# Performance work log

Hardware: AMD Instinct MI355X
Metric: run time of the kernel (lower is better)

Reference implementation:

```python
import jax, jax.numpy as jnp
import numpy as np

HEAD_DIM = 128
N = 64  # board_size**2


def setup_inputs() -> dict:
    key = jax.random.key(0)
    ks = jax.random.split(key, 14)
    B, C = 64, 256
    d = HEAD_DIM
    sc_conv = (2.0 / d) ** 0.5          # kaiming fan_out for 1x1 conv (fan_out = out_ch)
    inp = {
        'x': jax.random.normal(ks[0], (B, C, 8, 8), dtype=jnp.float32),
        # 1x1 convs stored as [out, in] matrices
        'w_src': jax.random.normal(ks[1], (d, C), dtype=jnp.float32) * sc_conv,
        'b_src': jax.random.normal(ks[2], (d,), dtype=jnp.float32) * 0.01,
        'w_dst': jax.random.normal(ks[3], (d, C), dtype=jnp.float32) * sc_conv,
        'b_dst': jax.random.normal(ks[4], (d,), dtype=jnp.float32) * 0.01,
        'w_arr': jax.random.normal(ks[5], (d, C), dtype=jnp.float32) * sc_conv,
        'b_arr': jax.random.normal(ks[6], (d,), dtype=jnp.float32) * 0.01,
        # move_fusion MLP: Linear(256,256) -> ReLU -> Linear(256,128) -> ReLU -> Linear(128,128)
        'w1': jax.random.normal(ks[7], (2 * d, 2 * d), dtype=jnp.float32) * (2.0 / (2 * d)) ** 0.5,
        'b1': jnp.zeros((2 * d,), dtype=jnp.float32),
        'w2': jax.random.normal(ks[8], (d, 2 * d), dtype=jnp.float32) * (2.0 / d) ** 0.5,
        'b2': jnp.zeros((d,), dtype=jnp.float32),
        'w3': jax.random.normal(ks[9], (d, d), dtype=jnp.float32) * (2.0 / d) ** 0.5,
        'b3': jnp.zeros((d,), dtype=jnp.float32),
    }
    return inp


def reference(x, w_src, b_src, w_dst, b_dst, w_arr, b_arr, w1, b1, w2, b2, w3, b3):
    B, C, H, W = x.shape
    d = HEAD_DIM
    scale = 1.0 / d ** 0.5
    xf = x.reshape(B, C, N)                                   # B,C,64
    f_src = jnp.einsum('oc,bcn->bon', w_src, xf) + b_src[:, None]  # B,128,64
    f_dst = jnp.einsum('oc,bcn->bon', w_dst, xf) + b_dst[:, None]
    f_arr = jnp.einsum('oc,bcn->bon', w_arr, xf) + b_arr[:, None]

    q_src = jnp.transpose(f_src, (0, 2, 1))                   # B,N,128
    move_logits = jnp.einsum('bnd,bdm->bnm', q_src, f_dst) * scale  # B,N,N

    # Linear(cat([v_src, v_dst])) decomposed: v@W1^T = src@W1[:, :d]^T + dst@W1[:, d:]^T
    dst_t = jnp.transpose(f_dst, (0, 2, 1))                   # B,N,128
    src_p = jnp.einsum('bnd,hd->bnh', q_src, w1[:, :d])       # B,N,256
    dst_p = jnp.einsum('bmd,hd->bmh', dst_t, w1[:, d:])       # B,N,256
    h1 = jax.nn.relu(src_p[:, :, None, :] + dst_p[:, None, :, :] + b1)  # B,N,N,256
    h2 = jax.nn.relu(jnp.einsum('bnmh,oh->bnmo', h1, w2) + b2)          # B,N,N,128
    q = jnp.einsum('bnmo,po->bnmp', h2, w3) + b3                        # B,N,N,128
    arrow_logits = jnp.einsum('bnmd,bdk->bnmk', q, f_arr).reshape(B, N * N, N) * scale
    return (move_logits, arrow_logits)
```

## Files before the change

### kernel.cpp

```cpp
#include <hip/hip_runtime.h>
#include <hip/hip_bf16.h>
#include <cstdint>

#define DEV __device__ __forceinline__

typedef __bf16 bf16_t;
typedef __bf16 bf16x8 __attribute__((ext_vector_type(8)));
typedef __bf16 bf16x4 __attribute__((ext_vector_type(4)));
typedef float  f32x4  __attribute__((ext_vector_type(4)));

constexpr float SCALE = 0.08838834764831845f;

constexpr size_t OFF_WSRC = 0;
constexpr size_t OFF_WDST = 65536;
constexpr size_t OFF_WARR = 131072;
constexpr size_t OFF_W1   = 196608;
constexpr size_t OFF_W2   = 327680;
constexpr size_t OFF_W3T  = 393216;
constexpr size_t OFF_FT   = 425984;
constexpr size_t OFF_GT   = OFF_FT + 3u*1048576u;
constexpr size_t OFF_C    = OFF_GT + 1048576u;
constexpr size_t OFF_SP   = OFF_C + 16384u;
constexpr size_t OFF_DP   = OFF_SP + 4194304u;

DEV f32x4 mfma16(bf16x8 a, bf16x8 b, f32x4 c) {
  return __builtin_amdgcn_mfma_f32_16x16x32_bf16(a, b, c, 0, 0, 0);
}

DEV bf16x8 lds_ld8(const bf16_t* base, int row, int k, int ldaBytes) {
  int off = (row * ldaBytes + k * 2) ^ ((row & 7) << 4);
  return *(const bf16x8*)((const char*)base + off);
}
DEV void lds_st8(bf16_t* base, int row, int k, int ldaBytes, bf16x8 v) {
  int off = (row * ldaBytes + k * 2) ^ ((row & 7) << 4);
  *(bf16x8*)((char*)base + off) = v;
}
DEV void lds_st4(bf16_t* base, int row, int k, int ldaBytes, bf16x4 v) {
  int off = (row * ldaBytes + k * 2) ^ ((row & 7) << 4);
  *(bf16x4*)((char*)base + off) = v;
}
DEV void lds_st1(bf16_t* base, int row, int k, int ldaBytes, bf16_t v) {
  int off = (row * ldaBytes + k * 2) ^ ((row & 7) << 4);
  *(bf16_t*)((char*)base + off) = v;
}
DEV bf16x8 g_ld8(const bf16_t* p) { return *(const bf16x8*)p; }

__global__ __launch_bounds__(256) void k0_prep(
    const float* __restrict__ wsrc, const float* __restrict__ wdst,
    const float* __restrict__ warr, const float* __restrict__ w1,
    const float* __restrict__ w2, const float* __restrict__ w3,
    char* __restrict__ ws)
{
  int tid = blockIdx.x * 256 + threadIdx.x;
  int stride = gridDim.x * 256;
  bf16_t* osrc = (bf16_t*)(ws + OFF_WSRC);
  bf16_t* odst = (bf16_t*)(ws + OFF_WDST);
  bf16_t* oarr = (bf16_t*)(ws + OFF_WARR);
  bf16_t* ow1  = (bf16_t*)(ws + OFF_W1);
  bf16_t* ow2  = (bf16_t*)(ws + OFF_W2);
  bf16_t* ow3t = (bf16_t*)(ws + OFF_W3T);
  for (int i = tid; i < 32768; i += stride) {
    osrc[i] = (bf16_t)wsrc[i];
    odst[i] = (bf16_t)wdst[i];
    oarr[i] = (bf16_t)warr[i];
    ow2[i]  = (bf16_t)w2[i];
  }
  for (int i = tid; i < 65536; i += stride) ow1[i] = (bf16_t)w1[i];
  for (int i = tid; i < 16384; i += stride) {
    int o = i >> 7, p = i & 127;
    ow3t[i] = (bf16_t)w3[p * 128 + o];
  }
}

__global__ __launch_bounds__(256) void k1_fproj(
    const float* __restrict__ x,
    const float* __restrict__ bsrc, const float* __restrict__ bdst,
    const float* __restrict__ barr, char* __restrict__ ws)
{
  int X = blockIdx.x % 3, b = blockIdx.x / 3;
  __shared__ __attribute__((aligned(16))) bf16_t xfT[64 * 256];

  int t = threadIdx.x;
  const float* xb = x + (size_t)b * 16384;
  #pragma unroll
  for (int i = 0; i < 16; i++) {
    int idx4 = (i * 256 + t) * 4;
    int c = idx4 >> 6, p = idx4 & 63;
    f32x4 v = *(const f32x4*)(xb + idx4);
    #pragma unroll
    for (int j = 0; j < 4; j++) lds_st1(xfT, p + j, c, 512, (bf16_t)v[j]);
  }
  __syncthreads();

  const bf16_t* wb = (const bf16_t*)(ws + OFF_WSRC + (size_t)X * 65536);
  const float* bias = (X == 0) ? bsrc : ((X == 1) ? bdst : barr);
  bf16_t* fT = (bf16_t*)(ws + OFF_FT + (size_t)X * 1048576u + (size_t)b * 16384u);

  int lane = t & 63, wave = t >> 6, r16 = lane & 15, g = lane >> 4;
  f32x4 z = {0.f, 0.f, 0.f, 0.f};
  f32x4 acc[2][4];
  #pragma unroll
  for (int rf = 0; rf < 2; rf++)
    #pragma unroll
    for (int cf = 0; cf < 4; cf++) acc[rf][cf] = z;

  #pragma unroll
  for (int ks = 0; ks < 8; ks++) {
    int k = ks * 32 + g * 8;
    bf16x8 a[2], bb[4];
    #pragma unroll
    for (int rf = 0; rf < 2; rf++)
      a[rf] = g_ld8(wb + (wave * 32 + rf * 16 + r16) * 256 + k);
    #pragma unroll
    for (int cf = 0; cf < 4; cf++) bb[cf] = lds_ld8(xfT, cf * 16 + r16, k, 512);
    __builtin_amdgcn_s_setprio(1);
    #pragma unroll
    for (int rf = 0; rf < 2; rf++)
      #pragma unroll
      for (int cf = 0; cf < 4; cf++) acc[rf][cf] = mfma16(a[rf], bb[cf], acc[rf][cf]);
    __builtin_amdgcn_s_setprio(0);
  }
  #pragma unroll
  for (int rf = 0; rf < 2; rf++) {
    int o0 = wave * 32 + rf * 16 + g * 4;
    f32x4 bv = *(const f32x4*)(bias + o0);
    #pragma unroll
    for (int cf = 0; cf < 4; cf++) {
      int p = cf * 16 + r16;
      bf16x4 pk;
      #pragma unroll
      for (int j = 0; j < 4; j++) pk[j] = (bf16_t)(acc[rf][cf][j] + bv[j]);
      *(bf16x4*)(fT + p * 128 + o0) = pk;
    }
  }
}

__global__ __launch_bounds__(256) void k2_pre(
    const float* __restrict__ b1, const float* __restrict__ b3,
    char* __restrict__ ws, float* __restrict__ out)
{
  int b = blockIdx.x & 63, task = blockIdx.x >> 6;
  int t = threadIdx.x, lane = t & 63, wave = t >> 6, r16 = lane & 15, g = lane >> 4;
  const bf16_t* fsrcT = (const bf16_t*)(ws + OFF_FT) + (size_t)b * 8192;
  const bf16_t* fdstT = (const bf16_t*)(ws + OFF_FT + 1048576u) + (size_t)b * 8192;
  const bf16_t* farrT = (const bf16_t*)(ws + OFF_FT + 2097152u) + (size_t)b * 8192;
  f32x4 z = {0.f, 0.f, 0.f, 0.f};

  if (task == 0) {
    f32x4 acc[4];
    #pragma unroll
    for (int cf = 0; cf < 4; cf++) acc[cf] = z;
    #pragma unroll
    for (int ks = 0; ks < 4; ks++) {
      int k = ks * 32 + g * 8;
      bf16x8 bb = g_ld8(fsrcT + (wave * 16 + r16) * 128 + k);
      #pragma unroll
      for (int cf = 0; cf < 4; cf++) {
        bf16x8 a = g_ld8(fdstT + (cf * 16 + r16) * 128 + k);
        acc[cf] = mfma16(a, bb, acc[cf]);
      }
    }
    float* ob = out + (size_t)b * 4096;
    int n = wave * 16 + r16;
    #pragma unroll
    for (int cf = 0; cf < 4; cf++) {
      f32x4 v;
      #pragma unroll
      for (int j = 0; j < 4; j++) v[j] = acc[cf][j] * SCALE;
      *(f32x4*)(ob + n * 64 + cf * 16 + g * 4) = v;
    }
  } else if (task <= 2) {
    const bf16_t* Bm = (const bf16_t*)(ws + OFF_W1) + (size_t)(wave * 64) * 256 + (task == 2 ? 128 : 0);
    const bf16_t* A = (task == 1) ? fsrcT : fdstT;
    f32x4 acc[4][4];
    #pragma unroll
    for (int cf = 0; cf < 4; cf++)
      #pragma unroll
      for (int rf = 0; rf < 4; rf++) acc[cf][rf] = z;
    #pragma unroll
    for (int ks = 0; ks < 4; ks++) {
      int k = ks * 32 + g * 8;
      bf16x8 aw[4], bb[4];
      #pragma unroll
      for (int cf = 0; cf < 4; cf++) aw[cf] = g_ld8(Bm + (cf * 16 + r16) * 256 + k);
      #pragma unroll
      for (int rf = 0; rf < 4; rf++) bb[rf] = g_ld8(A + (rf * 16 + r16) * 128 + k);
      __builtin_amdgcn_s_setprio(1);
      #pragma unroll
      for (int cf = 0; cf < 4; cf++)
        #pragma unroll
        for (int rf = 0; rf < 4; rf++) acc[cf][rf] = mfma16(aw[cf], bb[rf], acc[cf][rf]);
      __builtin_amdgcn_s_setprio(0);
    }
    if (task == 1) {
      float* sp = (float*)(ws + OFF_SP) + (size_t)b * 16384;
      #pragma unroll
      for (int cf = 0; cf < 4; cf++) {
        int h0 = wave * 64 + cf * 16 + g * 4;
        f32x4 bv = *(const f32x4*)(b1 + h0);
        #pragma unroll
        for (int rf = 0; rf < 4; rf++) {
          int n = rf * 16 + r16;
          *(f32x4*)(sp + n * 256 + h0) = acc[cf][rf] + bv;
        }
      }
    } else {
      bf16_t* dpo = (bf16_t*)(ws + OFF_DP) + (size_t)b * 16384;
      #pragma unroll
      for (int cf = 0; cf < 4; cf++) {
        int h0 = wave * 64 + cf * 16 + g * 4;
        #pragma unroll
        for (int rf = 0; rf < 4; rf++) {
          int m = rf * 16 + r16;
          bf16x4 pk;
          #pragma unroll
          for (int j = 0; j < 4; j++) pk[j] = (bf16_t)acc[cf][rf][j];
          *(bf16x4*)(dpo + m * 256 + h0) = pk;
        }
      }
    }
  } else {
    const bf16_t* A = (const bf16_t*)(ws + OFF_W3T) + (size_t)(wave * 32) * 128;
    f32x4 acc[2][4];
    #pragma unroll
    for (int rf = 0; rf < 2; rf++)
      #pragma unroll
      for (int cf = 0; cf < 4; cf++) acc[rf][cf] = z;
    #pragma unroll
    for (int ks = 0; ks < 4; ks++) {
      int k = ks * 32 + g * 8;
      bf16x8 a[2], bb[4];
      #pragma unroll
      for (int rf = 0; rf < 2; rf++) a[rf] = g_ld8(A + (rf * 16 + r16) * 128 + k);
      #pragma unroll
      for (int cf = 0; cf < 4; cf++) bb[cf] = g_ld8(farrT + (cf * 16 + r16) * 128 + k);
      #pragma unroll
      for (int rf = 0; rf < 2; rf++)
        #pragma unroll
        for (int cf = 0; cf < 4; cf++) acc[rf][cf] = mfma16(a[rf], bb[cf], acc[rf][cf]);
    }
    bf16_t* GT = (bf16_t*)(ws + OFF_GT) + (size_t)b * 8192;
    #pragma unroll
    for (int rf = 0; rf < 2; rf++) {
      int o0 = wave * 32 + rf * 16 + g * 4;
      #pragma unroll
      for (int cf = 0; cf < 4; cf++) {
        int kc = cf * 16 + r16;
        bf16x4 pk;
        #pragma unroll
        for (int j = 0; j < 4; j++) pk[j] = (bf16_t)(acc[rf][cf][j] * SCALE);
        *(bf16x4*)(GT + kc * 128 + o0) = pk;
      }
    }
    if (t < 64) {
      float s = 0.f;
      for (int p = 0; p < 128; p++) s += b3[p] * (float)farrT[t * 128 + p];
      ((float*)(ws + OFF_C))[b * 64 + t] = s * SCALE;
    }
  }
}

__global__ __launch_bounds__(512, 2) void k3_main(
    const float* __restrict__ b2, const char* __restrict__ ws, float* __restrict__ out)
{
  int p = blockIdx.x;
  int l = (p & 7) * 32 + (p >> 3);
  int b = l >> 2, nq = l & 3;

  __shared__ __attribute__((aligned(16))) bf16_t h1[2][64 * 256];
  __shared__ __attribute__((aligned(16))) bf16_t h2[2][64 * 128];
  __shared__ __attribute__((aligned(16))) float  spL[16 * 256];

  int t = threadIdx.x, lane = t & 63, w = t >> 6, r16 = lane & 15, g = lane >> 4;
  int mt = w & 3;
  int mh = w >> 2;

  const bf16_t* dp  = (const bf16_t*)(ws + OFF_DP) + (size_t)b * 16384;
  const float*  spg = (const float*)(ws + OFF_SP) + ((size_t)b * 64 + nq * 16) * 256;
  const bf16_t* w2b = (const bf16_t*)(ws + OFF_W2);
  const bf16_t* GTb = (const bf16_t*)(ws + OFF_GT) + (size_t)b * 8192;

  {
    f32x4 a0 = *(const f32x4*)(spg + t * 8);
    f32x4 a1 = *(const f32x4*)(spg + t * 8 + 4);
    *(f32x4*)(spL + t * 8)     = a0;
    *(f32x4*)(spL + t * 8 + 4) = a1;
  }
  bf16x8 dpr[4];
  #pragma unroll
  for (int ks = 0; ks < 4; ks++)
    dpr[ks] = g_ld8(dp + (mt * 16 + r16) * 256 + (mh * 4 + ks) * 32 + g * 8);
  bf16x8 w2r[4][8];
  #pragma unroll
  for (int ot = 0; ot < 4; ot++)
    #pragma unroll
    for (int ks = 0; ks < 8; ks++)
      w2r[ot][ks] = g_ld8(w2b + ((mh * 4 + ot) * 16 + r16) * 256 + ks * 32 + g * 8);
  bf16x8 gtr[4];
  #pragma unroll
  for (int ks = 0; ks < 4; ks++)
    gtr[ks] = g_ld8(GTb + (mt * 16 + r16) * 128 + ks * 32 + g * 8);
  f32x4 b2v[4];
  #pragma unroll
  for (int ot = 0; ot < 4; ot++)
    b2v[ot] = *(const f32x4*)(b2 + (mh * 4 + ot) * 16 + g * 4);
  f32x4 cvv = *(const f32x4*)((const float*)(ws + OFF_C) + b * 64 + mt * 16 + g * 4);
  f32x4 z = {0.f, 0.f, 0.f, 0.f};

  __syncthreads();

  {
    int row = mt * 16 + r16;
    #pragma unroll
    for (int ks = 0; ks < 4; ks++) {
      int k = (mh * 4 + ks) * 32 + g * 8;
      f32x4 s0 = *(const f32x4*)(spL + k);
      f32x4 s1 = *(const f32x4*)(spL + k + 4);
      bf16x8 hv;
      #pragma unroll
      for (int j = 0; j < 8; j++) {
        float v = (float)dpr[ks][j] + (j < 4 ? s0[j] : s1[j - 4]);
        hv[j] = (bf16_t)fmaxf(v, 0.f);
      }
      lds_st8(h1[0], row, k, 512, hv);
    }
  }
  __syncthreads();

  float* ob_base = out + 262144u + ((size_t)(b * 64 + nq * 16)) * 4096u;

  for (int nn = 0; nn < 16; ++nn) {
    int cur = nn & 1, nxt = cur ^ 1;

    if (nn < 15) {
      int row = mt * 16 + r16;
      const float* spn = spL + (nn + 1) * 256;
      #pragma unroll
      for (int ks = 0; ks < 4; ks++) {
        int k = (mh * 4 + ks) * 32 + g * 8;
        f32x4 s0 = *(const f32x4*)(spn + k);
        f32x4 s1 = *(const f32x4*)(spn + k + 4);
        bf16x8 hv;
        #pragma unroll
        for (int j = 0; j < 8; j++) {
          float v = (float)dpr[ks][j] + (j < 4 ? s0[j] : s1[j - 4]);
          hv[j] = (bf16_t)fmaxf(v, 0.f);
        }
        lds_st8(h1[nxt], row, k, 512, hv);
      }
    }

    f32x4 acc[4];
    #pragma unroll
    for (int ot = 0; ot < 4; ot++) acc[ot] = z;
    #pragma unroll
    for (int ks = 0; ks < 8; ks++) {
      bf16x8 bb = lds_ld8(h1[cur], mt * 16 + r16, ks * 32 + g * 8, 512);
      __builtin_amdgcn_s_setprio(1);
      #pragma unroll
      for (int ot = 0; ot < 4; ot++) acc[ot] = mfma16(w2r[ot][ks], bb, acc[ot]);
      __builtin_amdgcn_s_setprio(0);
    }

    #pragma unroll
    for (int ot = 0; ot < 4; ot++) {
      int o0 = (mh * 4 + ot) * 16 + g * 4;
      bf16x4 pk;
      #pragma unroll
      for (int j = 0; j < 4; j++) pk[j] = (bf16_t)fmaxf(acc[ot][j] + b2v[ot][j], 0.f);
      lds_st4(h2[cur], mt * 16 + r16, o0, 256, pk);
    }

    __syncthreads();

    f32x4 acc2[2];
    #pragma unroll
    for (int i = 0; i < 2; i++) acc2[i] = z;
    #pragma unroll
    for (int ks = 0; ks < 4; ks++) {
      __builtin_amdgcn_s_setprio(1);
      #pragma unroll
      for (int i = 0; i < 2; i++) {
        bf16x8 bb = lds_ld8(h2[cur], (mh * 2 + i) * 16 + r16, ks * 32 + g * 8, 256);
        acc2[i] = mfma16(gtr[ks], bb, acc2[i]);
      }
      __builtin_amdgcn_s_setprio(0);
    }
    float* ob = ob_base + (size_t)nn * 4096u;
    #pragma unroll
    for (int i = 0; i < 2; i++) {
      int m = (mh * 2 + i) * 16 + r16;
      *(f32x4*)(ob + m * 64 + mt * 16 + g * 4) = acc2[i] + cvv;
    }
  }
}

extern "C" void kernel_launch(void* const* d_in, const int* in_sizes, int n_in,
                              void* d_out, int out_size, void* d_ws, size_t ws_size,
                              hipStream_t stream) {
  (void)in_sizes; (void)n_in; (void)out_size; (void)ws_size;
  const float* x    = (const float*)d_in[0];
  const float* wsrc = (const float*)d_in[1];
  const float* bsrc = (const float*)d_in[2];
  const float* wdst = (const float*)d_in[3];
  const float* bdst = (const float*)d_in[4];
  const float* warr = (const float*)d_in[5];
  const float* barr = (const float*)d_in[6];
  const float* w1   = (const float*)d_in[7];
  const float* b1   = (const float*)d_in[8];
  const float* w2   = (const float*)d_in[9];
  const float* b2   = (const float*)d_in[10];
  const float* w3   = (const float*)d_in[11];
  const float* b3   = (const float*)d_in[12];
  char* ws = (char*)d_ws;
  float* out = (float*)d_out;

  hipLaunchKernelGGL(k0_prep, dim3(64), dim3(256), 0, stream, wsrc, wdst, warr, w1, w2, w3, ws);
  hipLaunchKernelGGL(k1_fproj, dim3(192), dim3(256), 0, stream, x, bsrc, bdst, barr, ws);
  hipLaunchKernelGGL(k2_pre, dim3(256), dim3(256), 0, stream, b1, b3, ws, out);
  hipLaunchKernelGGL(k3_main, dim3(256), dim3(512), 0, stream, b2, ws, out);
}
```

Measured before the change: 66.23 us.

## Halve per-block rows, single-buffer LDS and double grid for occupancy

Each k3 block now processes 8 source rows instead of 16, doubling the grid to 512 blocks. The double-buffered h1/h2 LDS arrays become single buffers, roughly halving shared memory so more blocks can be resident, and launch bounds ask for 4 blocks per SM. In exchange, overlap between h1 construction and the MFMA stage is lost, an extra barrier is added per iteration, per-block weight register loads are amortised over fewer rows, and the tighter register bound may cause spills.

```diff
diff --git a/kernel.cpp b/kernel.cpp
--- a/kernel.cpp
+++ b/kernel.cpp
@@ -260,36 +260,33 @@
   }
 }
 
-__global__ __launch_bounds__(512, 2) void k3_main(
+__global__ __launch_bounds__(512, 4) void k3_main(
     const float* __restrict__ b2, const char* __restrict__ ws, float* __restrict__ out)
 {
   int p = blockIdx.x;
-  int l = (p & 7) * 32 + (p >> 3);
-  int b = l >> 2, nq = l & 3;
-
-  __shared__ __attribute__((aligned(16))) bf16_t h1[2][64 * 256];
-  __shared__ __attribute__((aligned(16))) bf16_t h2[2][64 * 128];
-  __shared__ __attribute__((aligned(16))) float  spL[16 * 256];
+  int l = (p & 7) * 64 + (p >> 3);
+  int b = l >> 3, ne = l & 7;
+
+  __shared__ __attribute__((aligned(16))) bf16_t h1[64 * 256];
+  __shared__ __attribute__((aligned(16))) bf16_t h2[64 * 128];
+  __shared__ __attribute__((aligned(16))) float  spL[8 * 256];
 
   int t = threadIdx.x, lane = t & 63, w = t >> 6, r16 = lane & 15, g = lane >> 4;
   int mt = w & 3;
   int mh = w >> 2;
 
   const bf16_t* dp  = (const bf16_t*)(ws + OFF_DP) + (size_t)b * 16384;
-  const float*  spg = (const float*)(ws + OFF_SP) + ((size_t)b * 64 + nq * 16) * 256;
+  const float*  spg = (const float*)(ws + OFF_SP) + ((size_t)b * 64 + ne * 8) * 256;
   const bf16_t* w2b = (const bf16_t*)(ws + OFF_W2);
   const bf16_t* GTb = (const bf16_t*)(ws + OFF_GT) + (size_t)b * 8192;
 
-  {
-    f32x4 a0 = *(const f32x4*)(spg + t * 8);
-    f32x4 a1 = *(const f32x4*)(spg + t * 8 + 4);
-    *(f32x4*)(spL + t * 8)     = a0;
-    *(f32x4*)(spL + t * 8 + 4) = a1;
-  }
+  *(f32x4*)(spL + t * 4) = *(const f32x4*)(spg + t * 4);
+
+  int row = t >> 3, kq = t & 7;
   bf16x8 dpr[4];
   #pragma unroll
-  for (int ks = 0; ks < 4; ks++)
-    dpr[ks] = g_ld8(dp + (mt * 16 + r16) * 256 + (mh * 4 + ks) * 32 + g * 8);
+  for (int c8 = 0; c8 < 4; c8++)
+    dpr[c8] = g_ld8(dp + row * 256 + kq * 32 + c8 * 8);
   bf16x8 w2r[4][8];
   #pragma unroll
   for (int ot = 0; ot < 4; ot++)
@@ -309,68 +306,46 @@
 
   __syncthreads();
 
-  {
-    int row = mt * 16 + r16;
-    #pragma unroll
-    for (int ks = 0; ks < 4; ks++) {
-      int k = (mh * 4 + ks) * 32 + g * 8;
-      f32x4 s0 = *(const f32x4*)(spL + k);
-      f32x4 s1 = *(const f32x4*)(spL + k + 4);
-      bf16x8 hv;
-      #pragma unroll
-      for (int j = 0; j < 8; j++) {
-        float v = (float)dpr[ks][j] + (j < 4 ? s0[j] : s1[j - 4]);
-        hv[j] = (bf16_t)fmaxf(v, 0.f);
-      }
-      lds_st8(h1[0], row, k, 512, hv);
-    }
-  }
-  __syncthreads();
-
-  float* ob_base = out + 262144u + ((size_t)(b * 64 + nq * 16)) * 4096u;
-
-  for (int nn = 0; nn < 16; ++nn) {
-    int cur = nn & 1, nxt = cur ^ 1;
-
-    if (nn < 15) {
-      int row = mt * 16 + r16;
-      const float* spn = spL + (nn + 1) * 256;
-      #pragma unroll
-      for (int ks = 0; ks < 4; ks++) {
-        int k = (mh * 4 + ks) * 32 + g * 8;
+  float* ob_base = out + 262144u + ((size_t)(b * 64 + ne * 8)) * 4096u;
+
+  for (int nn = 0; nn < 8; ++nn) {
+    {
+      const float* spn = spL + nn * 256;
+      #pragma unroll
+      for (int c8 = 0; c8 < 4; c8++) {
+        int k = kq * 32 + c8 * 8;
         f32x4 s0 = *(const f32x4*)(spn + k);
         f32x4 s1 = *(const f32x4*)(spn + k + 4);
         bf16x8 hv;
         #pragma unroll
         for (int j = 0; j < 8; j++) {
-          float v = (float)dpr[ks][j] + (j < 4 ? s0[j] : s1[j - 4]);
+          float v = (float)dpr[c8][j] + (j < 4 ? s0[j] : s1[j - 4]);
           hv[j] = (bf16_t)fmaxf(v, 0.f);
         }
-        lds_st8(h1[nxt], row, k, 512, hv);
-      }
-    }
+        lds_st8(h1, row, k, 512, hv);
+      }
+    }
+    __syncthreads();
 
     f32x4 acc[4];
     #pragma unroll
     for (int ot = 0; ot < 4; ot++) acc[ot] = z;
     #pragma unroll
     for (int ks = 0; ks < 8; ks++) {
-      bf16x8 bb = lds_ld8(h1[cur], mt * 16 + r16, ks * 32 + g * 8, 512);
+      bf16x8 bb = lds_ld8(h1, mt * 16 + r16, ks * 32 + g * 8, 512);
       __builtin_amdgcn_s_setprio(1);
       #pragma unroll
       for (int ot = 0; ot < 4; ot++) acc[ot] = mfma16(w2r[ot][ks], bb, acc[ot]);
       __builtin_amdgcn_s_setprio(0);
     }
-
     #pragma unroll
     for (int ot = 0; ot < 4; ot++) {
       int o0 = (mh * 4 + ot) * 16 + g * 4;
       bf16x4 pk;
       #pragma unroll
       for (int j = 0; j < 4; j++) pk[j] = (bf16_t)fmaxf(acc[ot][j] + b2v[ot][j], 0.f);
-      lds_st4(h2[cur], mt * 16 + r16, o0, 256, pk);
-    }
-
+      lds_st4(h2, mt * 16 + r16, o0, 256, pk);
+    }
     __syncthreads();
 
     f32x4 acc2[2];
@@ -381,7 +356,7 @@
       __builtin_amdgcn_s_setprio(1);
       #pragma unroll
       for (int i = 0; i < 2; i++) {
-        bf16x8 bb = lds_ld8(h2[cur], (mh * 2 + i) * 16 + r16, ks * 32 + g * 8, 256);
+        bf16x8 bb = lds_ld8(h2, (mh * 2 + i) * 16 + r16, ks * 32 + g * 8, 256);
         acc2[i] = mfma16(gtr[ks], bb, acc2[i]);
       }
       __builtin_amdgcn_s_setprio(0);
@@ -418,5 +393,5 @@
   hipLaunchKernelGGL(k0_prep, dim3(64), dim3(256), 0, stream, wsrc, wdst, warr, w1, w2, w3, ws);
   hipLaunchKernelGGL(k1_fproj, dim3(192), dim3(256), 0, stream, x, bsrc, bdst, barr, ws);
   hipLaunchKernelGGL(k2_pre, dim3(256), dim3(256), 0, stream, b1, b3, ws, out);
-  hipLaunchKernelGGL(k3_main, dim3(256), dim3(512), 0, stream, b2, ws, out);
-}
+  hipLaunchKernelGGL(k3_main, dim3(512), dim3(512), 0, stream, b2, ws, out);
+}
```

After: 226.1 us. 241% more time.

## Double k3_main block to 1024 threads and stream W2 fragments from global

Applied to the files above, without the earlier changes.

The main h1→h2→arrow kernel now runs with 1024 threads per block, so each wave handles half as many output tiles in both MFMA stages. The W2 fragments are no longer kept resident in registers and are reloaded from global/L2 inside the k-loop on every iteration. This lowers register pressure to fit the larger block and spreads the work across more waves. In exchange it adds repeated global loads of W2 per row and makes each barrier span twice as many waves.

```diff
diff --git a/kernel.cpp b/kernel.cpp
--- a/kernel.cpp
+++ b/kernel.cpp
@@ -260,7 +260,7 @@
   }
 }
 
-__global__ __launch_bounds__(512, 2) void k3_main(
+__global__ __launch_bounds__(1024) void k3_main(
     const float* __restrict__ b2, const char* __restrict__ ws, float* __restrict__ out)
 {
   int p = blockIdx.x;
@@ -280,50 +280,38 @@
   const bf16_t* w2b = (const bf16_t*)(ws + OFF_W2);
   const bf16_t* GTb = (const bf16_t*)(ws + OFF_GT) + (size_t)b * 8192;
 
-  {
-    f32x4 a0 = *(const f32x4*)(spg + t * 8);
-    f32x4 a1 = *(const f32x4*)(spg + t * 8 + 4);
-    *(f32x4*)(spL + t * 8)     = a0;
-    *(f32x4*)(spL + t * 8 + 4) = a1;
-  }
-  bf16x8 dpr[4];
-  #pragma unroll
-  for (int ks = 0; ks < 4; ks++)
-    dpr[ks] = g_ld8(dp + (mt * 16 + r16) * 256 + (mh * 4 + ks) * 32 + g * 8);
-  bf16x8 w2r[4][8];
-  #pragma unroll
-  for (int ot = 0; ot < 4; ot++)
-    #pragma unroll
-    for (int ks = 0; ks < 8; ks++)
-      w2r[ot][ks] = g_ld8(w2b + ((mh * 4 + ot) * 16 + r16) * 256 + ks * 32 + g * 8);
+  *(f32x4*)(spL + t * 4) = *(const f32x4*)(spg + t * 4);
+
+  int row = t >> 4, kq = t & 15;
+  bf16x8 dpr[2];
+  #pragma unroll
+  for (int c8 = 0; c8 < 2; c8++)
+    dpr[c8] = g_ld8(dp + row * 256 + kq * 16 + c8 * 8);
   bf16x8 gtr[4];
   #pragma unroll
   for (int ks = 0; ks < 4; ks++)
     gtr[ks] = g_ld8(GTb + (mt * 16 + r16) * 128 + ks * 32 + g * 8);
-  f32x4 b2v[4];
-  #pragma unroll
-  for (int ot = 0; ot < 4; ot++)
-    b2v[ot] = *(const f32x4*)(b2 + (mh * 4 + ot) * 16 + g * 4);
+  f32x4 b2v[2];
+  #pragma unroll
+  for (int ot = 0; ot < 2; ot++)
+    b2v[ot] = *(const f32x4*)(b2 + (mh * 2 + ot) * 16 + g * 4);
   f32x4 cvv = *(const f32x4*)((const float*)(ws + OFF_C) + b * 64 + mt * 16 + g * 4);
   f32x4 z = {0.f, 0.f, 0.f, 0.f};
 
   __syncthreads();
 
-  {
-    int row = mt * 16 + r16;
-    #pragma unroll
-    for (int ks = 0; ks < 4; ks++) {
-      int k = (mh * 4 + ks) * 32 + g * 8;
-      f32x4 s0 = *(const f32x4*)(spL + k);
-      f32x4 s1 = *(const f32x4*)(spL + k + 4);
-      bf16x8 hv;
-      #pragma unroll
-      for (int j = 0; j < 8; j++) {
-        float v = (float)dpr[ks][j] + (j < 4 ? s0[j] : s1[j - 4]);
-        hv[j] = (bf16_t)fmaxf(v, 0.f);
-      }
-      lds_st8(h1[0], row, k, 512, hv);
-    }
+  #pragma unroll
+  for (int c8 = 0; c8 < 2; c8++) {
+    int k = kq * 16 + c8 * 8;
+    f32x4 s0 = *(const f32x4*)(spL + k);
+    f32x4 s1 = *(const f32x4*)(spL + k + 4);
+    bf16x8 hv;
+    #pragma unroll
+    for (int j = 0; j < 8; j++) {
+      float v = (float)dpr[c8][j] + (j < 4 ? s0[j] : s1[j - 4]);
+      hv[j] = (bf16_t)fmaxf(v, 0.f);
+    }
+    lds_st8(h1[0], row, k, 512, hv);
   }
   __syncthreads();
 
@@ -333,38 +321,41 @@
     int cur = nn & 1, nxt = cur ^ 1;
 
     if (nn < 15) {
-      int row = mt * 16 + r16;
       const float* spn = spL + (nn + 1) * 256;
       #pragma unroll
-      for (int ks = 0; ks < 4; ks++) {
-        int k = (mh * 4 + ks) * 32 + g * 8;
+      for (int c8 = 0; c8 < 2; c8++) {
+        int k = kq * 16 + c8 * 8;
         f32x4 s0 = *(const f32x4*)(spn + k);
         f32x4 s1 = *(const f32x4*)(spn + k + 4);
         bf16x8 hv;
         #pragma unroll
         for (int j = 0; j < 8; j++) {
-          float v = (float)dpr[ks][j] + (j < 4 ? s0[j] : s1[j - 4]);
+          float v = (float)dpr[c8][j] + (j < 4 ? s0[j] : s1[j - 4]);
           hv[j] = (bf16_t)fmaxf(v, 0.f);
         }
         lds_st8(h1[nxt], row, k, 512, hv);
       }
     }
 
-    f32x4 acc[4];
-    #pragma unroll
-    for (int ot = 0; ot < 4; ot++) acc[ot] = z;
+    f32x4 acc[2];
+    #pragma unroll
+    for (int ot = 0; ot < 2; ot++) acc[ot] = z;
     #pragma unroll
     for (int ks = 0; ks < 8; ks++) {
+      bf16x8 aw[2];
+      #pragma unroll
+      for (int ot = 0; ot < 2; ot++)
+        aw[ot] = g_ld8(w2b + ((mh * 2 + ot) * 16 + r16) * 256 + ks * 32 + g * 8);
       bf16x8 bb = lds_ld8(h1[cur], mt * 16 + r16, ks * 32 + g * 8, 512);
       __builtin_amdgcn_s_setprio(1);
       #pragma unroll
-      for (int ot = 0; ot < 4; ot++) acc[ot] = mfma16(w2r[ot][ks], bb, acc[ot]);
+      for (int ot = 0; ot < 2; ot++) acc[ot] = mfma16(aw[ot], bb, acc[ot]);
       __builtin_amdgcn_s_setprio(0);
     }
 
     #pragma unroll
-    for (int ot = 0; ot < 4; ot++) {
-      int o0 = (mh * 4 + ot) * 16 + g * 4;
+    for (int ot = 0; ot < 2; ot++) {
+      int o0 = (mh * 2 + ot) * 16 + g * 4;
       bf16x4 pk;
       #pragma unroll
       for (int j = 0; j < 4; j++) pk[j] = (bf16_t)fmaxf(acc[ot][j] + b2v[ot][j], 0.f);
@@ -373,25 +364,15 @@
 
     __syncthreads();
 
-    f32x4 acc2[2];
-    #pragma unroll
-    for (int i = 0; i < 2; i++) acc2[i] = z;
+    f32x4 acc2 = z;
     #pragma unroll
     for (int ks = 0; ks < 4; ks++) {
-      __builtin_amdgcn_s_setprio(1);
-      #pragma unroll
-      for (int i = 0; i < 2; i++) {
-        bf16x8 bb = lds_ld8(h2[cur], (mh * 2 + i) * 16 + r16, ks * 32 + g * 8, 256);
-        acc2[i] = mfma16(gtr[ks], bb, acc2[i]);
-      }
-      __builtin_amdgcn_s_setprio(0);
+      bf16x8 bb = lds_ld8(h2[cur], mh * 16 + r16, ks * 32 + g * 8, 256);
+      acc2 = mfma16(gtr[ks], bb, acc2);
     }
     float* ob = ob_base + (size_t)nn * 4096u;
-    #pragma unroll
-    for (int i = 0; i < 2; i++) {
-      int m = (mh * 2 + i) * 16 + r16;
-      *(f32x4*)(ob + m * 64 + mt * 16 + g * 4) = acc2[i] + cvv;
-    }
+    int m = mh * 16 + r16;
+    *(f32x4*)(ob + m * 64 + mt * 16 + g * 4) = acc2 + cvv;
   }
 }
 
@@ -418,5 +399,5 @@
   hipLaunchKernelGGL(k0_prep, dim3(64), dim3(256), 0, stream, wsrc, wdst, warr, w1, w2, w3, ws);
   hipLaunchKernelGGL(k1_fproj, dim3(192), dim3(256), 0, stream, x, bsrc, bdst, barr, ws);
   hipLaunchKernelGGL(k2_pre, dim3(256), dim3(256), 0, stream, b1, b3, ws, out);
-  hipLaunchKernelGGL(k3_main, dim3(256), dim3(512), 0, stream, b2, ws, out);
-}
+  hipLaunchKernelGGL(k3_main, dim3(256), dim3(1024), 0, stream, b2, ws, out);
+}
```

After: 91.08 us. 1.38x slower.

## Retile layer-2 MFMA to 2x2 output tiles per wave and stream G from global

Applied to the files above, without the earlier changes.

Changes the per-wave tiling of the h1×W2 GEMM from one m-tile by four o-tiles to two m-tiles by two o-tiles. This halves the W2 register footprint and reuses each loaded h1 fragment across two MFMAs. The h1 producer is remapped to a row/k-quarter thread layout. The G^T fragments are no longer kept in registers but are reloaded from global memory inside the inner loop. That cuts register pressure, which may improve occupancy or scheduling, but adds repeated global loads on every iteration.

```diff
diff --git a/kernel.cpp b/kernel.cpp
--- a/kernel.cpp
+++ b/kernel.cpp
@@ -272,8 +272,8 @@
   __shared__ __attribute__((aligned(16))) float  spL[16 * 256];
 
   int t = threadIdx.x, lane = t & 63, w = t >> 6, r16 = lane & 15, g = lane >> 4;
-  int mt = w & 3;
-  int mh = w >> 2;
+  int mo = w & 3;
+  int mm = w >> 2;
 
   const bf16_t* dp  = (const bf16_t*)(ws + OFF_DP) + (size_t)b * 16384;
   const float*  spg = (const float*)(ws + OFF_SP) + ((size_t)b * 64 + nq * 16) * 256;
@@ -286,44 +286,38 @@
     *(f32x4*)(spL + t * 8)     = a0;
     *(f32x4*)(spL + t * 8 + 4) = a1;
   }
+  int row = t >> 3, kq = t & 7;
   bf16x8 dpr[4];
   #pragma unroll
-  for (int ks = 0; ks < 4; ks++)
-    dpr[ks] = g_ld8(dp + (mt * 16 + r16) * 256 + (mh * 4 + ks) * 32 + g * 8);
-  bf16x8 w2r[4][8];
-  #pragma unroll
-  for (int ot = 0; ot < 4; ot++)
+  for (int c8 = 0; c8 < 4; c8++)
+    dpr[c8] = g_ld8(dp + row * 256 + kq * 32 + c8 * 8);
+  bf16x8 w2r[2][8];
+  #pragma unroll
+  for (int ot = 0; ot < 2; ot++)
     #pragma unroll
     for (int ks = 0; ks < 8; ks++)
-      w2r[ot][ks] = g_ld8(w2b + ((mh * 4 + ot) * 16 + r16) * 256 + ks * 32 + g * 8);
-  bf16x8 gtr[4];
-  #pragma unroll
-  for (int ks = 0; ks < 4; ks++)
-    gtr[ks] = g_ld8(GTb + (mt * 16 + r16) * 128 + ks * 32 + g * 8);
-  f32x4 b2v[4];
-  #pragma unroll
-  for (int ot = 0; ot < 4; ot++)
-    b2v[ot] = *(const f32x4*)(b2 + (mh * 4 + ot) * 16 + g * 4);
-  f32x4 cvv = *(const f32x4*)((const float*)(ws + OFF_C) + b * 64 + mt * 16 + g * 4);
+      w2r[ot][ks] = g_ld8(w2b + ((mo * 2 + ot) * 16 + r16) * 256 + ks * 32 + g * 8);
+  f32x4 b2v[2];
+  #pragma unroll
+  for (int ot = 0; ot < 2; ot++)
+    b2v[ot] = *(const f32x4*)(b2 + (mo * 2 + ot) * 16 + g * 4);
+  f32x4 cvv = *(const f32x4*)((const float*)(ws + OFF_C) + b * 64 + mo * 16 + g * 4);
   f32x4 z = {0.f, 0.f, 0.f, 0.f};
 
   __syncthreads();
 
-  {
-    int row = mt * 16 + r16;
-    #pragma unroll
-    for (int ks = 0; ks < 4; ks++) {
-      int k = (mh * 4 + ks) * 32 + g * 8;
-      f32x4 s0 = *(const f32x4*)(spL + k);
-      f32x4 s1 = *(const f32x4*)(spL + k + 4);
-      bf16x8 hv;
-      #pragma unroll
-      for (int j = 0; j < 8; j++) {
-        float v = (float)dpr[ks][j] + (j < 4 ? s0[j] : s1[j - 4]);
-        hv[j] = (bf16_t)fmaxf(v, 0.f);
-      }
-      lds_st8(h1[0], row, k, 512, hv);
-    }
+  #pragma unroll
+  for (int c8 = 0; c8 < 4; c8++) {
+    int k = kq * 32 + c8 * 8;
+    f32x4 s0 = *(const f32x4*)(spL + k);
+    f32x4 s1 = *(const f32x4*)(spL + k + 4);
+    bf16x8 hv;
+    #pragma unroll
+    for (int j = 0; j < 8; j++) {
+      float v = (float)dpr[c8][j] + (j < 4 ? s0[j] : s1[j - 4]);
+      hv[j] = (bf16_t)fmaxf(v, 0.f);
+    }
+    lds_st8(h1[0], row, k, 512, hv);
   }
   __syncthreads();
 
@@ -333,42 +327,53 @@
     int cur = nn & 1, nxt = cur ^ 1;
 
     if (nn < 15) {
-      int row = mt * 16 + r16;
       const float* spn = spL + (nn + 1) * 256;
       #pragma unroll
-      for (int ks = 0; ks < 4; ks++) {
-        int k = (mh * 4 + ks) * 32 + g * 8;
+      for (int c8 = 0; c8 < 4; c8++) {
+        int k = kq * 32 + c8 * 8;
         f32x4 s0 = *(const f32x4*)(spn + k);
         f32x4 s1 = *(const f32x4*)(spn + k + 4);
         bf16x8 hv;
         #pragma unroll
         for (int j = 0; j < 8; j++) {
-          float v = (float)dpr[ks][j] + (j < 4 ? s0[j] : s1[j - 4]);
+          float v = (float)dpr[c8][j] + (j < 4 ? s0[j] : s1[j - 4]);
           hv[j] = (bf16_t)fmaxf(v, 0.f);
         }
         lds_st8(h1[nxt], row, k, 512, hv);
       }
     }
 
-    f32x4 acc[4];
-    #pragma unroll
-    for (int ot = 0; ot < 4; ot++) acc[ot] = z;
+    f32x4 acc[2][2];
+    #pragma unroll
+    for (int ot = 0; ot < 2; ot++)
+      #pragma unroll
+      for (int mi = 0; mi < 2; mi++) acc[ot][mi] = z;
     #pragma unroll
     for (int ks = 0; ks < 8; ks++) {
-      bf16x8 bb = lds_ld8(h1[cur], mt * 16 + r16, ks * 32 + g * 8, 512);
+      bf16x8 bb[2];
+      #pragma unroll
+      for (int mi = 0; mi < 2; mi++)
+        bb[mi] = lds_ld8(h1[cur], (mm * 2 + mi) * 16 + r16, ks * 32 + g * 8, 512);
       __builtin_amdgcn_s_setprio(1);
       #pragma unroll
-      for (int ot = 0; ot < 4; ot++) acc[ot] = mfma16(w2r[ot][ks], bb, acc[ot]);
+      for (int ot = 0; ot < 2; ot++)
+        #pragma unroll
+        for (int mi = 0; mi < 2; mi++)
+          acc[ot][mi] = mfma16(w2r[ot][ks], bb[mi], acc[ot][mi]);
       __builtin_amdgcn_s_setprio(0);
     }
 
     #pragma unroll
-    for (int ot = 0; ot < 4; ot++) {
-      int o0 = (mh * 4 + ot) * 16 + g * 4;
-      bf16x4 pk;
-      #pragma unroll
-      for (int j = 0; j < 4; j++) pk[j] = (bf16_t)fmaxf(acc[ot][j] + b2v[ot][j], 0.f);
-      lds_st4(h2[cur], mt * 16 + r16, o0, 256, pk);
+    for (int ot = 0; ot < 2; ot++) {
+      int o0 = (mo * 2 + ot) * 16 + g * 4;
+      #pragma unroll
+      for (int mi = 0; mi < 2; mi++) {
+        int m = (mm * 2 + mi) * 16 + r16;
+        bf16x4 pk;
+        #pragma unroll
+        for (int j = 0; j < 4; j++) pk[j] = (bf16_t)fmaxf(acc[ot][mi][j] + b2v[ot][j], 0.f);
+        lds_st4(h2[cur], m, o0, 256, pk);
+      }
     }
 
     __syncthreads();
@@ -378,19 +383,20 @@
     for (int i = 0; i < 2; i++) acc2[i] = z;
     #pragma unroll
     for (int ks = 0; ks < 4; ks++) {
+      bf16x8 gt = g_ld8(GTb + (mo * 16 + r16) * 128 + ks * 32 + g * 8);
       __builtin_amdgcn_s_setprio(1);
       #pragma unroll
       for (int i = 0; i < 2; i++) {
-        bf16x8 bb = lds_ld8(h2[cur], (mh * 2 + i) * 16 + r16, ks * 32 + g * 8, 256);
-        acc2[i] = mfma16(gtr[ks], bb, acc2[i]);
+        bf16x8 bb = lds_ld8(h2[cur], (mm * 2 + i) * 16 + r16, ks * 32 + g * 8, 256);
+        acc2[i] = mfma16(gt, bb, acc2[i]);
       }
       __builtin_amdgcn_s_setprio(0);
     }
     float* ob = ob_base + (size_t)nn * 4096u;
     #pragma unroll
     for (int i = 0; i < 2; i++) {
-      int m = (mh * 2 + i) * 16 + r16;
-      *(f32x4*)(ob + m * 64 + mt * 16 + g * 4) = acc2[i] + cvv;
+      int m = (mm * 2 + i) * 16 + r16;
+      *(f32x4*)(ob + m * 64 + mo * 16 + g * 4) = acc2[i] + cvv;
     }
   }
 }
```

Measured after the change: 69.06 us. +4.3%, slower.
